# Kernel optimization log

Hardware: AMD Instinct MI355X
Metric: run time of the kernel (lower is better)

## Reference

```python
import jax, jax.numpy as jnp
import numpy as np

B, T, D = 2, 2048, 1024
H, W = 16, 256  # n_head, window_size
HD = D // H


def setup_inputs() -> dict:
    key = jax.random.key(0)
    ks = jax.random.split(key, 5)
    s = 0.02
    return {
        "x": jax.random.normal(ks[0], (B, T, D), dtype=jnp.float32),
        "Wqkv": jax.random.normal(ks[1], (3 * D, D), dtype=jnp.float32) * s,
        "bqkv": jax.random.normal(ks[2], (3 * D,), dtype=jnp.float32) * s,
        "Wo": jax.random.normal(ks[3], (D, D), dtype=jnp.float32) * s,
        "bo": jax.random.normal(ks[4], (D,), dtype=jnp.float32) * s,
    }


def reference(x, Wqkv, bqkv, Wo, bo):
    b, t, d = x.shape
    qkv = x @ Wqkv.T + bqkv  # [b, t, 3d]
    # rearrange 'b t (c h d) -> c b h t d'
    qkv = qkv.reshape(b, t, 3, H, HD)
    q = jnp.transpose(qkv[:, :, 0], (0, 2, 1, 3))  # [b, h, t, hd]
    k = jnp.transpose(qkv[:, :, 1], (0, 2, 1, 3))
    v = jnp.transpose(qkv[:, :, 2], (0, 2, 1, 3))
    scores = jnp.einsum('bhid,bhjd->bhij', q, k) / jnp.sqrt(jnp.float32(HD))
    i = jnp.arange(t)[:, None]
    j = jnp.arange(t)[None, :]
    # tril(diag=0) & triu(diag=-(W-1)): j <= i and j >= i - (W-1)
    mask = (j <= i) & (j >= i - (W - 1))
    scores = jnp.where(mask, scores, -jnp.inf)
    probs = jax.nn.softmax(scores, axis=-1)
    y = jnp.einsum('bhij,bhjd->bhid', probs, v)
    y = jnp.transpose(y, (0, 2, 1, 3)).reshape(b, t, d)  # b h t d -> b t (h d)
    return y @ Wo.T + bo
```

## Files before the change

### kernel.cpp

```cpp
#include <hip/hip_runtime.h>
#include <hip/hip_bf16.h>
#include <stdint.h>


typedef __attribute__((ext_vector_type(8))) short short8;
typedef __attribute__((ext_vector_type(4))) float f32x4;

#define MFMA16(a, b, c) __builtin_amdgcn_mfma_f32_16x16x32_bf16((a), (b), (c), 0, 0, 0)

static __device__ __forceinline__ void gl_lds16(const void* g, void* l) {
  __builtin_amdgcn_global_load_lds(
      (const __attribute__((address_space(1))) unsigned int*)g,
      (__attribute__((address_space(3))) unsigned int*)l, 16, 0, 0);
}

#define LGKM0 do { asm volatile("s_waitcnt lgkmcnt(0)" ::: "memory"); \
                   __builtin_amdgcn_sched_barrier(0); } while (0)
#define BARM do { asm volatile("" ::: "memory"); \
                  __builtin_amdgcn_s_barrier(); \
                  asm volatile("" ::: "memory"); } while (0)

static __device__ __forceinline__ uint32_t pkbf(float x, float y) {
  union { __hip_bfloat16 h; uint16_t u; } a, b;
  a.h = __float2bfloat16(x);
  b.h = __float2bfloat16(y);
  return (uint32_t)a.u | ((uint32_t)b.u << 16);
}

__global__ void cvt_all(const float* __restrict__ x, const float* __restrict__ wqkv,
                        const float* __restrict__ wo, __hip_bfloat16* __restrict__ xb,
                        __hip_bfloat16* __restrict__ wqkvb,
                        __hip_bfloat16* __restrict__ wob) {
  const int N0 = 524288, N1 = 393216, N2 = 131072;
  int i = blockIdx.x * blockDim.x + threadIdx.x;
  const int stride = gridDim.x * blockDim.x;
  for (; i < N0 + N1 + N2; i += stride) {
    const float* in;
    __hip_bfloat16* out;
    int gidx;
    if (i < N0) { in = x; out = xb; gidx = i; }
    else if (i < N0 + N1) { in = wqkv; out = wqkvb; gidx = i - N0; }
    else { in = wo; out = wob; gidx = i - N0 - N1; }
    const float4* p = (const float4*)in + (size_t)gidx * 2;
    float4 v0 = p[0], v1 = p[1];
    union { short8 s; __hip_bfloat16 h[8]; } u;
    u.h[0] = __float2bfloat16(v0.x); u.h[1] = __float2bfloat16(v0.y);
    u.h[2] = __float2bfloat16(v0.z); u.h[3] = __float2bfloat16(v0.w);
    u.h[4] = __float2bfloat16(v1.x); u.h[5] = __float2bfloat16(v1.y);
    u.h[6] = __float2bfloat16(v1.z); u.h[7] = __float2bfloat16(v1.w);
    ((short8*)out)[gidx] = u.s;
  }
}

__global__ __launch_bounds__(512) void gemm_qkv(
    const __hip_bfloat16* __restrict__ A, const __hip_bfloat16* __restrict__ Bm,
    const float* __restrict__ bias,
    __hip_bfloat16* __restrict__ qb, __hip_bfloat16* __restrict__ kb,
    __hip_bfloat16* __restrict__ vt2) {
  __shared__ alignas(128) char smem[114688];
  const int tid = threadIdx.x;
  const int lane = tid & 63, w = tid >> 6;
  const int wm = w >> 2, wn = w & 3;
  const int r = lane & 15, g = lane >> 4;
  const int K = 1024, NT = 16;

  const int cpx = gridDim.x >> 3;
  const int swzb = (blockIdx.x & 7) * cpx + (blockIdx.x >> 3);
  const int bm = swzb >> 4, bn = swzb & 15;

  const int srow = tid >> 3;
  const int e = (tid & 7) ^ ((tid >> 4) & 7);
  const int koff = (e >> 2) * 32 + (e & 3) * 8;
  const __hip_bfloat16* aU[4];
  const __hip_bfloat16* bU[3];
#pragma unroll
  for (int U = 0; U < 4; ++U)
    aU[U] = A + (size_t)(bm * 256 + U * 64 + srow) * K + koff;
#pragma unroll
  for (int U = 0; U < 3; ++U)
    bU[U] = Bm + (size_t)(bn * 192 + U * 64 + srow) * K + koff;
  const int ldst = tid * 16;

#define STA(t, U) gl_lds16(aU[U] + (t) * 64, smem + ((t) & 1) * 57344 + (U) * 8192 + ldst)
#define STB(t, U) gl_lds16(bU[U] + (t) * 64, smem + ((t) & 1) * 57344 + 32768 + (U) * 8192 + ldst)

  const int hsw = (r >> 1) & 7;
  const int s0 = ((0 + g) ^ hsw) * 16;
  const int s1 = ((4 + g) ^ hsw) * 16;
  const int rdA = (wm * 128 + r) * 128;
  const int rdB = 32768 + (wn * 48 + r) * 128;

  f32x4 acc[8][3] = {};
  short8 a0[4][2], a1[4][2], bb[3][2];

#pragma unroll
  for (int U = 0; U < 4; ++U) STA(0, U);
#pragma unroll
  for (int U = 0; U < 3; ++U) STB(0, U);
#pragma unroll
  for (int U = 0; U < 4; ++U) STA(1, U);
#pragma unroll
  for (int U = 0; U < 3; ++U) STB(1, U);
  asm volatile("s_waitcnt vmcnt(7)" ::: "memory");
  BARM;

#pragma unroll 1
  for (int t = 0; t < NT; ++t) {
    const char* cb = smem + (t & 1) * 57344;
#pragma unroll
    for (int i = 0; i < 4; ++i) {
      a0[i][0] = *(const short8*)(cb + rdA + i * 2048 + s0);
      a0[i][1] = *(const short8*)(cb + rdA + i * 2048 + s1);
    }
#pragma unroll
    for (int j = 0; j < 2; ++j) {
      bb[j][0] = *(const short8*)(cb + rdB + j * 2048 + s0);
      bb[j][1] = *(const short8*)(cb + rdB + j * 2048 + s1);
    }
    BARM;
    LGKM0;
    __builtin_amdgcn_s_setprio(1);
#pragma unroll
    for (int i = 0; i < 4; ++i)
#pragma unroll
      for (int j = 0; j < 2; ++j) acc[i][j] = MFMA16(a0[i][0], bb[j][0], acc[i][j]);
#pragma unroll
    for (int i = 0; i < 4; ++i)
#pragma unroll
      for (int j = 0; j < 2; ++j) acc[i][j] = MFMA16(a0[i][1], bb[j][1], acc[i][j]);
    __builtin_amdgcn_s_setprio(0);
    BARM;
#pragma unroll
    for (int i = 0; i < 4; ++i) {
      a1[i][0] = *(const short8*)(cb + rdA + (i + 4) * 2048 + s0);
      a1[i][1] = *(const short8*)(cb + rdA + (i + 4) * 2048 + s1);
    }
    BARM;
    LGKM0;
    __builtin_amdgcn_s_setprio(1);
#pragma unroll
    for (int i = 0; i < 4; ++i)
#pragma unroll
      for (int j = 0; j < 2; ++j) acc[i + 4][j] = MFMA16(a1[i][0], bb[j][0], acc[i + 4][j]);
#pragma unroll
    for (int i = 0; i < 4; ++i)
#pragma unroll
      for (int j = 0; j < 2; ++j) acc[i + 4][j] = MFMA16(a1[i][1], bb[j][1], acc[i + 4][j]);
    __builtin_amdgcn_s_setprio(0);
    BARM;
    bb[2][0] = *(const short8*)(cb + rdB + 2 * 2048 + s0);
    bb[2][1] = *(const short8*)(cb + rdB + 2 * 2048 + s1);
    if (t + 2 < NT) {
      STA(t + 2, 0); STA(t + 2, 1); STA(t + 2, 2); STA(t + 2, 3);
    }
    BARM;
    LGKM0;
    __builtin_amdgcn_s_setprio(1);
#pragma unroll
    for (int i = 0; i < 4; ++i) acc[i + 4][2] = MFMA16(a1[i][0], bb[2][0], acc[i + 4][2]);
#pragma unroll
    for (int i = 0; i < 4; ++i) acc[i + 4][2] = MFMA16(a1[i][1], bb[2][1], acc[i + 4][2]);
    __builtin_amdgcn_s_setprio(0);
    BARM;
    if (t + 2 < NT) {
      STB(t + 2, 0); STB(t + 2, 1); STB(t + 2, 2);
    }
    BARM;
    __builtin_amdgcn_s_setprio(1);
#pragma unroll
    for (int i = 0; i < 4; ++i) acc[i][2] = MFMA16(a0[i][0], bb[2][0], acc[i][2]);
#pragma unroll
    for (int i = 0; i < 4; ++i) acc[i][2] = MFMA16(a0[i][1], bb[2][1], acc[i][2]);
    __builtin_amdgcn_s_setprio(0);
    if (t + 2 < NT) {
      asm volatile("s_waitcnt vmcnt(7)" ::: "memory");
    } else if (t + 1 < NT) {
      asm volatile("s_waitcnt vmcnt(0)" ::: "memory");
    }
    BARM;
  }
#undef STA
#undef STB

  float bjv[3];
  const int nb = bn * 192 + wn * 48;
#pragma unroll
  for (int j = 0; j < 3; ++j) bjv[j] = bias[nb + j * 16 + r];
#pragma unroll
  for (int i = 0; i < 8; ++i) {
    const int m0 = bm * 256 + wm * 128 + i * 16 + g * 4;
#pragma unroll
    for (int j = 0; j < 3; ++j) {
      const int nn = nb + j * 16 + r;
      const int c = nn >> 10, h = (nn >> 6) & 15, hd = nn & 63;
      const int b_ = m0 >> 11, t0 = m0 & 2047;
      const size_t hb = (size_t)(b_ * 16 + h);
      if (c == 0) {
#pragma unroll
        for (int q = 0; q < 4; ++q)
          qb[(hb * 2048 + t0 + q) * 64 + hd] =
              __float2bfloat16((acc[i][j][q] + bjv[j]) * 0.125f);
      } else if (c == 1) {
#pragma unroll
        for (int q = 0; q < 4; ++q)
          kb[(hb * 2048 + t0 + q) * 64 + hd] =
              __float2bfloat16(acc[i][j][q] + bjv[j]);
      } else {
        union { uint2 u; __hip_bfloat16 hh[4]; } pk;
#pragma unroll
        for (int q = 0; q < 4; ++q)
          pk.hh[q] = __float2bfloat16(acc[i][j][q] + bjv[j]);
        const int kk = t0 & 31;
        const int pp = ((kk & 12) << 1) + ((kk & 16) >> 2);
        *(uint2*)&vt2[hb * 131072 + (size_t)(t0 >> 5) * 2048 + hd * 32 + pp] =
            pk.u;
      }
    }
  }
}

__global__ __launch_bounds__(256) void gemm_bt_out(
    const __hip_bfloat16* __restrict__ A, const __hip_bfloat16* __restrict__ Bm,
    const float* __restrict__ bias, float* __restrict__ outF, int K, int nbn) {
  __shared__ alignas(16) __hip_bfloat16 As[128 * 32];
  __shared__ alignas(16) __hip_bfloat16 Bs[128 * 32];
  const int bm = blockIdx.x / nbn, bn = blockIdx.x % nbn;
  const int tid = threadIdx.x;
  const int lane = tid & 63, w = tid >> 6;
  const int wr = w >> 1, wc = w & 1;
  const int r = lane & 15, g = lane >> 4;

  f32x4 acc[4][4] = {};

  const int c0 = tid, c1 = tid + 256;
  const __hip_bfloat16* a0 = A + (size_t)(bm * 128 + (c0 >> 2)) * K + (c0 & 3) * 8;
  const __hip_bfloat16* a1 = A + (size_t)(bm * 128 + (c1 >> 2)) * K + (c1 & 3) * 8;
  const __hip_bfloat16* b0 = Bm + (size_t)(bn * 128 + (c0 >> 2)) * K + (c0 & 3) * 8;
  const __hip_bfloat16* b1 = Bm + (size_t)(bn * 128 + (c1 >> 2)) * K + (c1 & 3) * 8;
  __hip_bfloat16* la0 = &As[c0 * 8];
  __hip_bfloat16* la1 = &As[c1 * 8];
  __hip_bfloat16* lb0 = &Bs[c0 * 8];
  __hip_bfloat16* lb1 = &Bs[c1 * 8];

  for (int k0 = 0; k0 < K; k0 += 32) {
    gl_lds16(a0 + k0, la0);
    gl_lds16(a1 + k0, la1);
    gl_lds16(b0 + k0, lb0);
    gl_lds16(b1 + k0, lb1);
    __syncthreads();
    short8 af[4], bf[4];
#pragma unroll
    for (int i = 0; i < 4; ++i)
      af[i] = *(const short8*)&As[(wr * 64 + i * 16 + r) * 32 + g * 8];
#pragma unroll
    for (int j = 0; j < 4; ++j)
      bf[j] = *(const short8*)&Bs[(wc * 64 + j * 16 + r) * 32 + g * 8];
#pragma unroll
    for (int i = 0; i < 4; ++i)
#pragma unroll
      for (int j = 0; j < 4; ++j) acc[i][j] = MFMA16(af[i], bf[j], acc[i][j]);
    __syncthreads();
  }

#pragma unroll
  for (int i = 0; i < 4; ++i) {
    const int mbase = bm * 128 + wr * 64 + i * 16 + g * 4;
#pragma unroll
    for (int j = 0; j < 4; ++j) {
      const int nn = bn * 128 + wc * 64 + j * 16 + r;
      const float bv = bias[nn];
#pragma unroll
      for (int q = 0; q < 4; ++q)
        outF[(size_t)(mbase + q) * 1024 + nn] = acc[i][j][q] + bv;
    }
  }
}

__global__ __launch_bounds__(512, 2) void attn_local(
    const __hip_bfloat16* __restrict__ qb, const __hip_bfloat16* __restrict__ kb,
    const __hip_bfloat16* __restrict__ vt2, __hip_bfloat16* __restrict__ yb) {
  __shared__ alignas(16) char smem[49152];
  const int xcd = blockIdx.x & 7;
  const int idx = blockIdx.x >> 3;
  const int bh = xcd + (idx >> 4) * 8;
  const int qt = idx & 15;
  const int tid = threadIdx.x;
  const int w = tid >> 6, lane = tid & 63;
  const int r = lane & 15, g = lane >> 4;
  const int qa = qt * 128 + w * 16;

  const __hip_bfloat16* qp = qb + (size_t)bh * 2048 * 64;
  const __hip_bfloat16* kp = kb + (size_t)bh * 2048 * 64;
  const __hip_bfloat16* vpb = vt2 + (size_t)bh * 131072 + r * 32 + g * 8;

  const int t_lo = (qt >= 2) ? (4 * qt - 8) : 0;
  const int t_hi = 4 * qt + 3;
  const int nunits = (t_hi - t_lo + 1) << 8;
  short8 stg[6];
#pragma unroll
  for (int rr = 0; rr < 6; ++rr) {
    const int u = rr * 512 + tid;
    if (u < nunits) {
      const int tt = u >> 8, row = (u >> 3) & 31, sl = u & 7;
      stg[rr] = *(const short8*)&kp[(size_t)((t_lo + tt) * 32 + row) * 64 + sl * 8];
    }
  }
#pragma unroll
  for (int rr = 0; rr < 6; ++rr) {
    const int u = rr * 512 + tid;
    if (u < nunits) {
      const int tt = u >> 8, row = (u >> 3) & 31, sl = u & 7;
      *(short8*)(smem + tt * 4096 + row * 128 + ((sl ^ (row & 7)) << 4)) = stg[rr];
    }
  }
  __syncthreads();

  const short8 qf0 = *(const short8*)&qp[(qa + r) * 64 + g * 8];
  const short8 qf1 = *(const short8*)&qp[(qa + r) * 64 + g * 8 + 32];

  f32x4 acc[4] = {};
  float m = -1e30f;
  float lsum = 0.f;

  const int wlo = ((qa >= 256) ? ((qa - 255) >> 5) : 0) - t_lo;
  const int whi = ((qa + 15) >> 5) - t_lo;
  const int xsw = (r & 7) << 4;

#pragma unroll 1
  for (int tt = wlo; tt <= whi; ++tt) {
    const int tabs = t_lo + tt;
    const int kbase = tabs << 5;
    const short8 v0 = *(const short8*)(vpb + (size_t)tabs * 2048);
    const short8 v1 = *(const short8*)(vpb + (size_t)tabs * 2048 + 512);
    const short8 v2 = *(const short8*)(vpb + (size_t)tabs * 2048 + 1024);
    const short8 v3 = *(const short8*)(vpb + (size_t)tabs * 2048 + 1536);
    const char* kt = smem + tt * 4096;
    const short8 k00 = *(const short8*)(kt + r * 128 + (((g) << 4) ^ xsw));
    const short8 k01 = *(const short8*)(kt + r * 128 + (((4 + g) << 4) ^ xsw));
    const short8 k10 = *(const short8*)(kt + (16 + r) * 128 + (((g) << 4) ^ xsw));
    const short8 k11 = *(const short8*)(kt + (16 + r) * 128 + (((4 + g) << 4) ^ xsw));
    f32x4 st0 = {}, st1 = {};
    st0 = MFMA16(k00, qf0, st0);
    st0 = MFMA16(k01, qf1, st0);
    st1 = MFMA16(k10, qf0, st1);
    st1 = MFMA16(k11, qf1, st1);
    float sv[2][4];
#pragma unroll
    for (int q = 0; q < 4; ++q) {
      const unsigned d0 = (unsigned)(qa + r) - (unsigned)(kbase + g * 4 + q);
      const unsigned d1 = (unsigned)(qa + r) - (unsigned)(kbase + 16 + g * 4 + q);
      sv[0][q] = (d0 <= 255u) ? st0[q] : -1e30f;
      sv[1][q] = (d1 <= 255u) ? st1[q] : -1e30f;
    }
    const float tmax = fmaxf(
        fmaxf(fmaxf(sv[0][0], sv[0][1]), fmaxf(sv[0][2], sv[0][3])),
        fmaxf(fmaxf(sv[1][0], sv[1][1]), fmaxf(sv[1][2], sv[1][3])));
    if (!__all(tmax <= m + 8.f)) {
      float rm = tmax;
      rm = fmaxf(rm, __shfl_xor(rm, 16));
      rm = fmaxf(rm, __shfl_xor(rm, 32));
      const float mnew = fmaxf(m, rm);
      const float fac = __expf(m - mnew);
      m = mnew;
      lsum *= fac;
      acc[0] *= fac; acc[1] *= fac; acc[2] *= fac; acc[3] *= fac;
    }
    float p[2][4];
#pragma unroll
    for (int f = 0; f < 2; ++f)
#pragma unroll
      for (int q = 0; q < 4; ++q) {
        p[f][q] = __expf(sv[f][q] - m);
        lsum += p[f][q];
      }
    union { short8 s; uint32_t u[4]; } pb;
    pb.u[0] = pkbf(p[0][0], p[0][1]);
    pb.u[1] = pkbf(p[0][2], p[0][3]);
    pb.u[2] = pkbf(p[1][0], p[1][1]);
    pb.u[3] = pkbf(p[1][2], p[1][3]);
    acc[0] = MFMA16(v0, pb.s, acc[0]);
    acc[1] = MFMA16(v1, pb.s, acc[1]);
    acc[2] = MFMA16(v2, pb.s, acc[2]);
    acc[3] = MFMA16(v3, pb.s, acc[3]);
  }

  lsum += __shfl_xor(lsum, 16);
  lsum += __shfl_xor(lsum, 32);
  const float inv = 1.f / lsum;

  const int b_ = bh >> 4, h = bh & 15;
  __hip_bfloat16* yrow = yb + (size_t)(b_ * 2048 + qa + r) * 1024 + h * 64;
#pragma unroll
  for (int u = 0; u < 4; ++u) {
    union { uint2 uu; __hip_bfloat16 hh[4]; } pk;
#pragma unroll
    for (int q = 0; q < 4; ++q) pk.hh[q] = __float2bfloat16(acc[u][q] * inv);
    *(uint2*)&yrow[u * 16 + g * 4] = pk.uu;
  }
}

extern "C" void kernel_launch(void* const* d_in, const int* in_sizes, int n_in,
                              void* d_out, int out_size, void* d_ws,
                              size_t ws_size, hipStream_t stream) {
  const float* x = (const float*)d_in[0];
  const float* Wqkv = (const float*)d_in[1];
  const float* bqkv = (const float*)d_in[2];
  const float* Wo = (const float*)d_in[3];
  const float* bo = (const float*)d_in[4];
  float* out = (float*)d_out;

  char* ws = (char*)d_ws;
  __hip_bfloat16* xb = (__hip_bfloat16*)(ws + 0);
  __hip_bfloat16* wqkvb = (__hip_bfloat16*)(ws + 8388608);
  __hip_bfloat16* wob = (__hip_bfloat16*)(ws + 14680064);
  __hip_bfloat16* qb = (__hip_bfloat16*)(ws + 16777216);
  __hip_bfloat16* kb = (__hip_bfloat16*)(ws + 25165824);
  __hip_bfloat16* vt2 = (__hip_bfloat16*)(ws + 33554432);
  __hip_bfloat16* yb = (__hip_bfloat16*)(ws + 41943040);

  cvt_all<<<2048, 256, 0, stream>>>(x, Wqkv, Wo, xb, wqkvb, wob);

  gemm_qkv<<<256, 512, 0, stream>>>(xb, wqkvb, bqkv, qb, kb, vt2);
  attn_local<<<512, 512, 0, stream>>>(qb, kb, vt2, yb);
  gemm_bt_out<<<256, 256, 0, stream>>>(yb, wob, bo, out, 1024, 8);
}
```

Measured before the change: 88.81 us.

## Rewrite output projection GEMM with 8-wave double-buffered pipelined K loop

Replaces the simple single-buffered output GEMM with an 8-wave, 512-thread kernel. It uses K=64 tiles double-buffered in LDS, XOR-swizzled LDS layout to avoid bank conflicts, XCD-aware block remapping, and interleaved global-to-LDS prefetch with MFMA phases under raised priority. The goal is to hide global load latency and the per-iteration sync stalls of the old loop. It adds complexity and hardcodes K and the grid shape, and uses more LDS per block.

After: 75.95 us. 14.5% less time.

```diff
diff --git a/kernel.cpp b/kernel.cpp
--- a/kernel.cpp
+++ b/kernel.cpp
@@ -219,59 +219,118 @@
   }
 }
 
-__global__ __launch_bounds__(256) void gemm_bt_out(
+__global__ __launch_bounds__(512, 4) void gemm_out8(
     const __hip_bfloat16* __restrict__ A, const __hip_bfloat16* __restrict__ Bm,
-    const float* __restrict__ bias, float* __restrict__ outF, int K, int nbn) {
-  __shared__ alignas(16) __hip_bfloat16 As[128 * 32];
-  __shared__ alignas(16) __hip_bfloat16 Bs[128 * 32];
-  const int bm = blockIdx.x / nbn, bn = blockIdx.x % nbn;
+    const float* __restrict__ bias, float* __restrict__ outF) {
+  __shared__ alignas(128) char smem[65536];
   const int tid = threadIdx.x;
   const int lane = tid & 63, w = tid >> 6;
-  const int wr = w >> 1, wc = w & 1;
+  const int wm = w >> 2, wn = w & 3;
   const int r = lane & 15, g = lane >> 4;
-
-  f32x4 acc[4][4] = {};
-
-  const int c0 = tid, c1 = tid + 256;
-  const __hip_bfloat16* a0 = A + (size_t)(bm * 128 + (c0 >> 2)) * K + (c0 & 3) * 8;
-  const __hip_bfloat16* a1 = A + (size_t)(bm * 128 + (c1 >> 2)) * K + (c1 & 3) * 8;
-  const __hip_bfloat16* b0 = Bm + (size_t)(bn * 128 + (c0 >> 2)) * K + (c0 & 3) * 8;
-  const __hip_bfloat16* b1 = Bm + (size_t)(bn * 128 + (c1 >> 2)) * K + (c1 & 3) * 8;
-  __hip_bfloat16* la0 = &As[c0 * 8];
-  __hip_bfloat16* la1 = &As[c1 * 8];
-  __hip_bfloat16* lb0 = &Bs[c0 * 8];
-  __hip_bfloat16* lb1 = &Bs[c1 * 8];
-
-  for (int k0 = 0; k0 < K; k0 += 32) {
-    gl_lds16(a0 + k0, la0);
-    gl_lds16(a1 + k0, la1);
-    gl_lds16(b0 + k0, lb0);
-    gl_lds16(b1 + k0, lb1);
-    __syncthreads();
-    short8 af[4], bf[4];
-#pragma unroll
-    for (int i = 0; i < 4; ++i)
-      af[i] = *(const short8*)&As[(wr * 64 + i * 16 + r) * 32 + g * 8];
-#pragma unroll
-    for (int j = 0; j < 4; ++j)
-      bf[j] = *(const short8*)&Bs[(wc * 64 + j * 16 + r) * 32 + g * 8];
-#pragma unroll
-    for (int i = 0; i < 4; ++i)
-#pragma unroll
-      for (int j = 0; j < 4; ++j) acc[i][j] = MFMA16(af[i], bf[j], acc[i][j]);
-    __syncthreads();
-  }
-
+  const int K = 1024, NT = 16;
+
+  const int cpx = gridDim.x >> 3;
+  const int swzb = (blockIdx.x & 7) * cpx + (blockIdx.x >> 3);
+  const int bm = swzb >> 3, bn = swzb & 7;
+
+  const int srow = tid >> 3;
+  const int e = (tid & 7) ^ ((tid >> 4) & 7);
+  const int koff = (e >> 2) * 32 + (e & 3) * 8;
+  const __hip_bfloat16* aU[2];
+  const __hip_bfloat16* bU[2];
+#pragma unroll
+  for (int U = 0; U < 2; ++U) {
+    aU[U] = A + (size_t)(bm * 128 + U * 64 + srow) * K + koff;
+    bU[U] = Bm + (size_t)(bn * 128 + U * 64 + srow) * K + koff;
+  }
+  const int ldst = tid * 16;
+
+#define STA(t, U) gl_lds16(aU[U] + (t) * 64, smem + ((t) & 1) * 32768 + (U) * 8192 + ldst)
+#define STB(t, U) gl_lds16(bU[U] + (t) * 64, smem + ((t) & 1) * 32768 + 16384 + (U) * 8192 + ldst)
+
+  const int hsw = (r >> 1) & 7;
+  const int s0 = ((0 + g) ^ hsw) * 16;
+  const int s1 = ((4 + g) ^ hsw) * 16;
+  const int rdA = (wm * 64 + r) * 128;
+  const int rdB = 16384 + (wn * 32 + r) * 128;
+
+  f32x4 acc[4][2] = {};
+  short8 af[4][2], bf[2][2];
+
+  STA(0, 0); STA(0, 1); STB(0, 0); STB(0, 1);
+  STA(1, 0); STA(1, 1); STB(1, 0); STB(1, 1);
+  asm volatile("s_waitcnt vmcnt(4)" ::: "memory");
+  BARM;
+
+#pragma unroll 1
+  for (int t = 0; t < NT; ++t) {
+    const char* cb = smem + (t & 1) * 32768;
+#pragma unroll
+    for (int i = 0; i < 2; ++i) {
+      af[i][0] = *(const short8*)(cb + rdA + i * 2048 + s0);
+      af[i][1] = *(const short8*)(cb + rdA + i * 2048 + s1);
+    }
+#pragma unroll
+    for (int j = 0; j < 2; ++j) {
+      bf[j][0] = *(const short8*)(cb + rdB + j * 2048 + s0);
+      bf[j][1] = *(const short8*)(cb + rdB + j * 2048 + s1);
+    }
+    BARM;
+    LGKM0;
+    __builtin_amdgcn_s_setprio(1);
+#pragma unroll
+    for (int i = 0; i < 2; ++i)
+#pragma unroll
+      for (int j = 0; j < 2; ++j) acc[i][j] = MFMA16(af[i][0], bf[j][0], acc[i][j]);
+#pragma unroll
+    for (int i = 0; i < 2; ++i)
+#pragma unroll
+      for (int j = 0; j < 2; ++j) acc[i][j] = MFMA16(af[i][1], bf[j][1], acc[i][j]);
+    __builtin_amdgcn_s_setprio(0);
+    BARM;
+#pragma unroll
+    for (int i = 0; i < 2; ++i) {
+      af[i + 2][0] = *(const short8*)(cb + rdA + (i + 2) * 2048 + s0);
+      af[i + 2][1] = *(const short8*)(cb + rdA + (i + 2) * 2048 + s1);
+    }
+    if (t + 2 < NT) { STB(t + 2, 0); STB(t + 2, 1); }
+    BARM;
+    LGKM0;
+    __builtin_amdgcn_s_setprio(1);
+#pragma unroll
+    for (int i = 0; i < 2; ++i)
+#pragma unroll
+      for (int j = 0; j < 2; ++j) acc[i + 2][j] = MFMA16(af[i + 2][0], bf[j][0], acc[i + 2][j]);
+#pragma unroll
+    for (int i = 0; i < 2; ++i)
+#pragma unroll
+      for (int j = 0; j < 2; ++j) acc[i + 2][j] = MFMA16(af[i + 2][1], bf[j][1], acc[i + 2][j]);
+    __builtin_amdgcn_s_setprio(0);
+    BARM;
+    if (t + 2 < NT) {
+      STA(t + 2, 0); STA(t + 2, 1);
+      asm volatile("s_waitcnt vmcnt(4)" ::: "memory");
+    } else if (t + 1 < NT) {
+      asm volatile("s_waitcnt vmcnt(0)" ::: "memory");
+    }
+    BARM;
+  }
+#undef STA
+#undef STB
+
+  float bjv[2];
+  const int nb = bn * 128 + wn * 32;
+#pragma unroll
+  for (int j = 0; j < 2; ++j) bjv[j] = bias[nb + j * 16 + r];
 #pragma unroll
   for (int i = 0; i < 4; ++i) {
-    const int mbase = bm * 128 + wr * 64 + i * 16 + g * 4;
-#pragma unroll
-    for (int j = 0; j < 4; ++j) {
-      const int nn = bn * 128 + wc * 64 + j * 16 + r;
-      const float bv = bias[nn];
+    const int m0 = bm * 128 + wm * 64 + i * 16 + g * 4;
+#pragma unroll
+    for (int j = 0; j < 2; ++j) {
+      const int nn = nb + j * 16 + r;
 #pragma unroll
       for (int q = 0; q < 4; ++q)
-        outF[(size_t)(mbase + q) * 1024 + nn] = acc[i][j][q] + bv;
+        outF[(size_t)(m0 + q) * 1024 + nn] = acc[i][j][q] + bjv[j];
     }
   }
 }
@@ -422,5 +481,5 @@
 
   gemm_qkv<<<256, 512, 0, stream>>>(xb, wqkvb, bqkv, qb, kb, vt2);
   attn_local<<<512, 512, 0, stream>>>(qb, kb, vt2, yb);
-  gemm_bt_out<<<256, 256, 0, stream>>>(yb, wob, bo, out, 1024, 8);
-}
+  gemm_out8<<<256, 512, 0, stream>>>(yb, wob, bo, out);
+}
```
